# Optimization experiments

Hardware: AMD Instinct MI355X
Metric: run time of the kernel (lower is better)

Reference implementation:

```python
import jax, jax.numpy as jnp
import numpy as np

NEG_SLOPE = 0.2
BN_EPS = 1e-5


def _gat_conv(x, src, dst, W, a_src, a_dst, b, n_nodes):
    # PyG GATConv, heads=1: linear, per-edge leaky-relu score, per-dst softmax, scatter-add.
    h = x @ W  # [N, C]
    e = jax.nn.leaky_relu((h @ a_src)[src] + (h @ a_dst)[dst], NEG_SLOPE)  # [E]
    m = jax.ops.segment_max(e, dst, num_segments=n_nodes)
    m = jnp.where(jnp.isfinite(m), m, 0.0)  # nodes with no in-edges
    w = jnp.exp(e - m[dst])
    denom = jax.ops.segment_sum(w, dst, num_segments=n_nodes)
    alpha = w / (denom[dst] + 1e-16)  # [E]
    out = jax.ops.segment_sum(alpha[:, None] * h[src], dst, num_segments=n_nodes)
    return out + b


def setup_inputs() -> dict:
    key = jax.random.key(0)
    N, E, Q, C = 50000, 800000, 200000, 128
    ks = jax.random.split(key, 12)
    sc = 1.0 / np.sqrt(C)
    d = {
        "embedding": jax.random.normal(ks[0], (N, C), jnp.float32) * 0.1,
        "W1": jax.random.normal(ks[1], (C, C), jnp.float32) * sc,
        "a_src1": jax.random.normal(ks[2], (C,), jnp.float32) * sc,
        "a_dst1": jax.random.normal(ks[3], (C,), jnp.float32) * sc,
        "b1": jnp.zeros((C,), jnp.float32),
        "gamma": jnp.ones((C,), jnp.float32),
        "beta": jnp.zeros((C,), jnp.float32),
        "rmean": jnp.zeros((C,), jnp.float32),
        "rvar": jnp.ones((C,), jnp.float32),
        "W2": jax.random.normal(ks[4], (C, C), jnp.float32) * sc,
        "a_src2": jax.random.normal(ks[5], (C,), jnp.float32) * sc,
        "a_dst2": jax.random.normal(ks[6], (C,), jnp.float32) * sc,
        "b2": jnp.zeros((C,), jnp.float32),
        "Wp1": jax.random.normal(ks[7], (C, C), jnp.float32) * sc,
        "bp1": jnp.zeros((C,), jnp.float32),
        "Wp2": jax.random.normal(ks[8], (C, 1), jnp.float32) * sc,
        "bp2": jnp.zeros((1,), jnp.float32),
        "edge_index": jax.random.randint(ks[9], (2, E), 0, N, jnp.int32),
        "edges": jax.random.randint(ks[10], (2, Q), 0, N, jnp.int32),
    }
    return d


def reference(embedding, W1, a_src1, a_dst1, b1, gamma, beta, rmean, rvar,
              W2, a_src2, a_dst2, b2, Wp1, bp1, Wp2, bp2, edge_index, edges):
    N = embedding.shape[0]
    src, dst = edge_index[0], edge_index[1]
    # conv0 -> BN (eval, running stats) -> ReLU (dropout inactive in eval)
    x = _gat_conv(embedding, src, dst, W1, a_src1, a_dst1, b1, N)
    x = (x - rmean) * jax.lax.rsqrt(rvar + BN_EPS) * gamma + beta
    x = jax.nn.relu(x)
    # final conv
    x = _gat_conv(x, src, dst, W2, a_src2, a_dst2, b2, N)
    # LinkPredictor: elementwise product of endpoint embeddings -> MLP -> sigmoid
    h = x[edges[0]] * x[edges[1]]  # [Q, C]
    h = jax.nn.relu(h @ Wp1 + bp1)
    out = jax.nn.sigmoid(h @ Wp2 + bp2)
    return out[:, 0]
```

## Files before the change

### kernel.cpp

```cpp
#include <hip/hip_runtime.h>
#include <hip/hip_bf16.h>
#include <math.h>
#include <stdint.h>
#include <string.h>

#define NEG_SLOPE 0.2f
#define BN_EPS 1e-5f

typedef __attribute__((ext_vector_type(8))) short short8;
typedef __attribute__((ext_vector_type(4))) float float4v;

static __device__ __forceinline__ unsigned short f2bf(float f) {
    union { float f; unsigned u; } v; v.f = f;
    unsigned r = (v.u + 0x7fffu + ((v.u >> 16) & 1u)) >> 16;
    return (unsigned short)r;
}
static __device__ __forceinline__ float bf2f(unsigned short u) {
    union { unsigned u; float f; } v; v.u = ((unsigned)u) << 16;
    return v.f;
}

__global__ __launch_bounds__(256) void prep_all(
    const float* __restrict__ W1, const float* __restrict__ W2,
    const float* __restrict__ Wp1,
    unsigned short* __restrict__ wt1, unsigned short* __restrict__ wt2,
    unsigned short* __restrict__ wtp,
    const float* __restrict__ gamma, const float* __restrict__ beta,
    const float* __restrict__ rmean, const float* __restrict__ rvar,
    float* __restrict__ bnsc, float* __restrict__ bnsh,
    int* __restrict__ bcur, int nb) {
    int b = blockIdx.x;
    if (b < 192) {
        const float* W = (b < 64) ? W1 : (b < 128) ? W2 : Wp1;
        unsigned short* WT = (b < 64) ? wt1 : (b < 128) ? wt2 : wtp;
        int idx = (b & 63) * 256 + threadIdx.x;
        int k = idx >> 7, n = idx & 127;
        WT[n * 128 + k] = f2bf(W[idx]);
    } else {
        if (threadIdx.x < 128) {
            int c = threadIdx.x;
            float s = gamma[c] * rsqrtf(rvar[c] + BN_EPS);
            bnsc[c] = s;
            bnsh[c] = beta[c] - rmean[c] * s;
        }
        for (int i = threadIdx.x; i < nb; i += 256) bcur[i] = 0;
    }
}

#define BK_CAP 8192
#define BK_EPB 4096
#define BK_LDS 6144

__global__ __launch_bounds__(256) void bucket_scatter(const int* __restrict__ src,
                                                      const int* __restrict__ dst,
                                                      int* __restrict__ bcur,
                                                      unsigned long long* __restrict__ bucket,
                                                      int E) {
    __shared__ int lcnt[256];
    __shared__ int lbase[256];
    int t = threadIdx.x;
    int e0 = blockIdx.x * BK_EPB;
    lcnt[t] = 0;
    __syncthreads();

    int es[16], ed[16];
#pragma unroll
    for (int u = 0; u < 16; ++u) {
        int i = e0 + u * 256 + t;
        if (i < E) {
            es[u] = src[i];
            ed[u] = dst[i];
            atomicAdd(&lcnt[ed[u] >> 8], 1);
        } else {
            ed[u] = -1;
        }
    }
    __syncthreads();
    int c = lcnt[t];
    if (c > 0) lbase[t] = atomicAdd(&bcur[t], c);
    __syncthreads();
    lcnt[t] = 0;
    __syncthreads();
#pragma unroll
    for (int u = 0; u < 16; ++u) {
        if (ed[u] >= 0) {
            int bin = ed[u] >> 8;
            int r = atomicAdd(&lcnt[bin], 1);
            int slot = lbase[bin] + r;
            if (slot < BK_CAP)
                bucket[(size_t)bin * BK_CAP + slot] =
                    ((unsigned long long)(ed[u] & 255) << 32) | (unsigned)es[u];
        }
    }
}

__global__ __launch_bounds__(1024) void scan_bucket_sums(const int* __restrict__ bcur,
                                                         int* __restrict__ bbase,
                                                         int* __restrict__ offs,
                                                         int nb, int N) {
    __shared__ int s[1024];
    int t = threadIdx.x;
    int v = 0;
    if (t < nb) { v = bcur[t]; if (v > BK_CAP) v = BK_CAP; }
    s[t] = v;
    __syncthreads();
    for (int d = 1; d < 1024; d <<= 1) {
        int u = (t >= d) ? s[t - d] : 0;
        __syncthreads();
        s[t] += u;
        __syncthreads();
    }
    if (t < nb) bbase[t] = s[t] - v;
    if (t == 1023) offs[N] = s[1023];
}

__global__ __launch_bounds__(256) void bucket_offs_fill(
    const int* __restrict__ bcur,
    const unsigned long long* __restrict__ bucket,
    const int* __restrict__ bbase,
    int* __restrict__ offs, int* __restrict__ csr, int N) {
    __shared__ unsigned long long rec[BK_LDS];
    __shared__ int cnt[256];
    __shared__ int sc[256];
    int t = threadIdx.x, b = blockIdx.x;
    const unsigned long long* gb = &bucket[(size_t)b * BK_CAP];
    cnt[t] = 0;
    int c = bcur[b];
    if (c > BK_CAP) c = BK_CAP;
    int lim = (c < BK_LDS) ? c : BK_LDS;
    for (int i = t; i < lim; i += 256) rec[i] = gb[i];
    __syncthreads();
    for (int i = t; i < c; i += 256) {
        unsigned long long v = (i < BK_LDS) ? rec[i] : gb[i];
        atomicAdd(&cnt[(int)(v >> 32)], 1);
    }
    __syncthreads();
    int v = cnt[t];
    sc[t] = v;
    __syncthreads();
    for (int d = 1; d < 256; d <<= 1) {
        int u = (t >= d) ? sc[t - d] : 0;
        __syncthreads();
        sc[t] += u;
        __syncthreads();
    }
    int myoff = bbase[b] + sc[t] - v;
    int node = (b << 8) + t;
    if (node < N) offs[node] = myoff;
    cnt[t] = myoff;
    __syncthreads();
    for (int i = t; i < c; i += 256) {
        unsigned long long rv = (i < BK_LDS) ? rec[i] : gb[i];
        int dl = (int)(rv >> 32);
        int s = (int)(rv & 0xffffffffu);
        int r = atomicAdd(&cnt[dl], 1);
        csr[r] = s;
    }
}

#define LP_RS 136

template <bool BF16_IN>
__global__ __launch_bounds__(256) void gemm_mfma(
    const void* __restrict__ Xv,
    const unsigned short* __restrict__ WT,
    const float* __restrict__ a_src, const float* __restrict__ a_dst,
    unsigned short* __restrict__ H,
    float* __restrict__ s_src, float* __restrict__ s_dst, int N)
{
    __shared__ unsigned short sA[128 * LP_RS];
    __shared__ unsigned short sW[128 * LP_RS];
    const float* Xf = (const float*)Xv;
    const unsigned short* Xh = (const unsigned short*)Xv;
    int tid = threadIdx.x;
    int r0 = blockIdx.x * 128;

#pragma unroll
    for (int it = 0; it < 8; ++it) {
        int idx = it * 2048 + tid * 8;
        int n = idx >> 7, k = idx & 127;
        *(short8*)&sW[n * LP_RS + k] = *(const short8*)&WT[idx];
    }
#pragma unroll
    for (int it = 0; it < 16; ++it) {
        int r = it * 8 + (tid >> 5);
        int c = (tid & 31) * 4;
        int row = r0 + r;
        ushort4 u = make_ushort4(0, 0, 0, 0);
        if (row < N) {
            if (BF16_IN) {
                u = *(const ushort4*)&Xh[(size_t)row * 128 + c];
            } else {
                float4 x = *(const float4*)&Xf[(size_t)row * 128 + c];
                u.x = f2bf(x.x); u.y = f2bf(x.y); u.z = f2bf(x.z); u.w = f2bf(x.w);
            }
        }
        *(ushort4*)&sA[r * LP_RS + c] = u;
    }
    __syncthreads();

    int wave = tid >> 6, lane = tid & 63;
    int ln = lane & 15, quad = lane >> 4;
    int rowbase = wave * 32;

    short8 af[2][4];
#pragma unroll
    for (int m = 0; m < 2; ++m)
#pragma unroll
        for (int kt = 0; kt < 4; ++kt)
            af[m][kt] = *(const short8*)&sA[(rowbase + m * 16 + ln) * LP_RS + kt * 32 + quad * 8];

    float4v acc[2][8];
#pragma unroll
    for (int m = 0; m < 2; ++m)
#pragma unroll
        for (int n = 0; n < 8; ++n)
            acc[m][n] = float4v{0.f, 0.f, 0.f, 0.f};

#pragma unroll
    for (int n = 0; n < 8; ++n) {
#pragma unroll
        for (int kt = 0; kt < 4; ++kt) {
            short8 bf = *(const short8*)&sW[(n * 16 + ln) * LP_RS + kt * 32 + quad * 8];
            acc[0][n] = __builtin_amdgcn_mfma_f32_16x16x32_bf16(af[0][kt], bf, acc[0][n], 0, 0, 0);
            acc[1][n] = __builtin_amdgcn_mfma_f32_16x16x32_bf16(af[1][kt], bf, acc[1][n], 0, 0, 0);
        }
    }

    float asr[8], adr[8];
#pragma unroll
    for (int n = 0; n < 8; ++n) {
        asr[n] = a_src[n * 16 + ln];
        adr[n] = a_dst[n * 16 + ln];
    }
#pragma unroll
    for (int m = 0; m < 2; ++m) {
        int rb = r0 + rowbase + m * 16 + quad * 4;
#pragma unroll
        for (int n = 0; n < 8; ++n) {
            int col = n * 16 + ln;
            float4v a = acc[m][n];
            if (rb + 0 < N) H[(size_t)(rb + 0) * 128 + col] = f2bf(a[0]);
            if (rb + 1 < N) H[(size_t)(rb + 1) * 128 + col] = f2bf(a[1]);
            if (rb + 2 < N) H[(size_t)(rb + 2) * 128 + col] = f2bf(a[2]);
            if (rb + 3 < N) H[(size_t)(rb + 3) * 128 + col] = f2bf(a[3]);
        }
#pragma unroll
        for (int r = 0; r < 4; ++r) {
            float ps = 0.f, pd = 0.f;
#pragma unroll
            for (int n = 0; n < 8; ++n) {
                float v = acc[m][n][r];
                ps = fmaf(v, asr[n], ps);
                pd = fmaf(v, adr[n], pd);
            }
#pragma unroll
            for (int o = 1; o < 16; o <<= 1) {
                ps += __shfl_xor(ps, o);
                pd += __shfl_xor(pd, o);
            }
            int row = rb + r;
            if (ln == 0 && row < N) { s_src[row] = ps; s_dst[row] = pd; }
        }
    }
}

__global__ __launch_bounds__(256) void edge_softmax(const int* __restrict__ off,
                                                    const int* __restrict__ csr,
                                                    const float* __restrict__ s_src,
                                                    const float* __restrict__ s_dst,
                                                    float* __restrict__ we,
                                                    float* __restrict__ invd, int N) {
    int tid = threadIdx.x;
    int node = blockIdx.x * 16 + (tid >> 4);
    if (node >= N) return;
    int ln = tid & 15;
    int beg = off[node], end = off[node + 1];
    float sd = s_dst[node];

    float sw = 0.f;
    for (int i = beg + ln; i < end; i += 16) {
        float e = s_src[csr[i]] + sd;
        e = (e >= 0.f) ? e : NEG_SLOPE * e;
        float w = expf(e);
        we[i] = w;
        sw += w;
    }
#pragma unroll
    for (int o = 8; o; o >>= 1) sw += __shfl_xor(sw, o);
    if (ln == 0) invd[node] = 1.f / (sw + 1e-16f);
}

__global__ __launch_bounds__(256) void gat_gather(const unsigned short* __restrict__ H,
                                                  const int* __restrict__ off,
                                                  const int* __restrict__ csr,
                                                  const float* __restrict__ we,
                                                  const float* __restrict__ invd,
                                                  const float* __restrict__ bias,
                                                  const float* __restrict__ bn_scale,
                                                  const float* __restrict__ bn_shift,
                                                  int do_bn_relu,
                                                  unsigned short* __restrict__ out, int N) {
    int wave = threadIdx.x >> 6, lane = threadIdx.x & 63;
    int half = lane >> 5, hl = lane & 31;
    int node = blockIdx.x * 8 + wave * 2 + half;
    if (node >= N) return;
    int c0 = hl * 4;
    int beg = off[node], end = off[node + 1];
    float inv = invd[node];

    float a0 = 0.f, a1 = 0.f, a2 = 0.f, a3 = 0.f;
    int i = beg;
    for (; i + 8 <= end; i += 8) {
        int s[8]; float w[8]; ushort4 hv[8];
#pragma unroll
        for (int u = 0; u < 8; ++u) { s[u] = csr[i + u]; w[u] = we[i + u]; }
#pragma unroll
        for (int u = 0; u < 8; ++u)
            hv[u] = *(const ushort4*)&H[(size_t)s[u] * 128 + c0];
#pragma unroll
        for (int u = 0; u < 8; ++u) {
            a0 = fmaf(w[u], bf2f(hv[u].x), a0);
            a1 = fmaf(w[u], bf2f(hv[u].y), a1);
            a2 = fmaf(w[u], bf2f(hv[u].z), a2);
            a3 = fmaf(w[u], bf2f(hv[u].w), a3);
        }
    }
    for (; i < end; ++i) {
        int s = csr[i];
        float w = we[i];
        ushort4 hv = *(const ushort4*)&H[(size_t)s * 128 + c0];
        a0 = fmaf(w, bf2f(hv.x), a0);
        a1 = fmaf(w, bf2f(hv.y), a1);
        a2 = fmaf(w, bf2f(hv.z), a2);
        a3 = fmaf(w, bf2f(hv.w), a3);
    }
    float o0 = a0 * inv + bias[c0 + 0];
    float o1 = a1 * inv + bias[c0 + 1];
    float o2 = a2 * inv + bias[c0 + 2];
    float o3 = a3 * inv + bias[c0 + 3];
    if (do_bn_relu) {
        o0 = fmaxf(o0 * bn_scale[c0 + 0] + bn_shift[c0 + 0], 0.f);
        o1 = fmaxf(o1 * bn_scale[c0 + 1] + bn_shift[c0 + 1], 0.f);
        o2 = fmaxf(o2 * bn_scale[c0 + 2] + bn_shift[c0 + 2], 0.f);
        o3 = fmaxf(o3 * bn_scale[c0 + 3] + bn_shift[c0 + 3], 0.f);
    }
    ushort4 ov;
    ov.x = f2bf(o0); ov.y = f2bf(o1); ov.z = f2bf(o2); ov.w = f2bf(o3);
    *(ushort4*)&out[(size_t)node * 128 + c0] = ov;
}

__global__ __launch_bounds__(512) void link_pred_mfma(
    const unsigned short* __restrict__ X,
    const int* __restrict__ E0, const int* __restrict__ E1,
    const unsigned short* __restrict__ WTg,
    const float* __restrict__ bp1,
    const float* __restrict__ Wp2,
    const float* __restrict__ bp2_p,
    float* __restrict__ out, int Q)
{
    __shared__ unsigned short sW[128 * LP_RS];
    int tid = threadIdx.x;
    int wave = tid >> 6, lane = tid & 63;
    int ln = lane & 15, quad = lane >> 4;

    int tile = blockIdx.x * 8 + wave;
    int qbase = tile * 32;

    int ea[2], eb[2];
#pragma unroll
    for (int m = 0; m < 2; ++m) {
        int q = qbase + m * 16 + ln;
        if (q >= Q) q = Q - 1;
        ea[m] = E0[q];
        eb[m] = E1[q];
    }

#pragma unroll
    for (int it = 0; it < 4; ++it) {
        int idx = it * 4096 + tid * 8;
        int n = idx >> 7, k = idx & 127;
        *(short8*)&sW[n * LP_RS + k] = *(const short8*)&WTg[idx];
    }

    short8 ra[2][4], rb[2][4];
#pragma unroll
    for (int m = 0; m < 2; ++m) {
        const unsigned short* pa = &X[(size_t)ea[m] * 128 + quad * 8];
        const unsigned short* pb = &X[(size_t)eb[m] * 128 + quad * 8];
#pragma unroll
        for (int kt = 0; kt < 4; ++kt) {
            ra[m][kt] = *(const short8*)(pa + kt * 32);
            rb[m][kt] = *(const short8*)(pb + kt * 32);
        }
    }

    float bias[8], w2c[8];
#pragma unroll
    for (int n = 0; n < 8; ++n) {
        bias[n] = bp1[n * 16 + ln];
        w2c[n] = Wp2[n * 16 + ln];
    }
    float b2 = bp2_p[0];

    __syncthreads();

    short8 af[2][4];
#pragma unroll
    for (int m = 0; m < 2; ++m) {
#pragma unroll
        for (int kt = 0; kt < 4; ++kt) {
            short8 p;
#pragma unroll
            for (int j = 0; j < 8; j += 2) {
                float p0 = bf2f((unsigned short)ra[m][kt][j]) *
                           bf2f((unsigned short)rb[m][kt][j]);
                float p1 = bf2f((unsigned short)ra[m][kt][j + 1]) *
                           bf2f((unsigned short)rb[m][kt][j + 1]);
                __hip_bfloat162 h2 = __float22bfloat162_rn(make_float2(p0, p1));
                unsigned pr;
                memcpy(&pr, &h2, 4);
                p[j]     = (short)(pr & 0xffffu);
                p[j + 1] = (short)(pr >> 16);
            }
            af[m][kt] = p;
        }
    }

    float r0[2] = {0.f, 0.f}, r1[2] = {0.f, 0.f}, r2[2] = {0.f, 0.f}, r3[2] = {0.f, 0.f};
#pragma unroll
    for (int n = 0; n < 8; ++n) {
        float4v a0 = float4v{bias[n], bias[n], bias[n], bias[n]};
        float4v a1 = a0;
#pragma unroll
        for (int kt = 0; kt < 4; ++kt) {
            short8 bf = *(const short8*)&sW[(n * 16 + ln) * LP_RS + kt * 32 + quad * 8];
            a0 = __builtin_amdgcn_mfma_f32_16x16x32_bf16(af[0][kt], bf, a0, 0, 0, 0);
            a1 = __builtin_amdgcn_mfma_f32_16x16x32_bf16(af[1][kt], bf, a1, 0, 0, 0);
        }
        float w = w2c[n];
        r0[0] += fmaxf(a0[0], 0.f) * w;  r0[1] += fmaxf(a1[0], 0.f) * w;
        r1[0] += fmaxf(a0[1], 0.f) * w;  r1[1] += fmaxf(a1[1], 0.f) * w;
        r2[0] += fmaxf(a0[2], 0.f) * w;  r2[1] += fmaxf(a1[2], 0.f) * w;
        r3[0] += fmaxf(a0[3], 0.f) * w;  r3[1] += fmaxf(a1[3], 0.f) * w;
    }
#pragma unroll
    for (int m = 0; m < 2; ++m) {
#pragma unroll
        for (int o = 1; o < 16; o <<= 1) {
            r0[m] += __shfl_xor(r0[m], o);
            r1[m] += __shfl_xor(r1[m], o);
            r2[m] += __shfl_xor(r2[m], o);
            r3[m] += __shfl_xor(r3[m], o);
        }
        if (ln == 0) {
            int rbase = qbase + m * 16 + quad * 4;
            float rv[4] = {r0[m], r1[m], r2[m], r3[m]};
#pragma unroll
            for (int r = 0; r < 4; ++r) {
                int q = rbase + r;
                if (q < Q) out[q] = 1.f / (1.f + expf(-(rv[r] + b2)));
            }
        }
    }
}

extern "C" void kernel_launch(void* const* d_in, const int* in_sizes, int n_in,
                              void* d_out, int out_size, void* d_ws, size_t ws_size,
                              hipStream_t stream) {
    const float* emb    = (const float*)d_in[0];
    const float* W1     = (const float*)d_in[1];
    const float* a_src1 = (const float*)d_in[2];
    const float* a_dst1 = (const float*)d_in[3];
    const float* b1     = (const float*)d_in[4];
    const float* gamma  = (const float*)d_in[5];
    const float* beta   = (const float*)d_in[6];
    const float* rmean  = (const float*)d_in[7];
    const float* rvar   = (const float*)d_in[8];
    const float* W2     = (const float*)d_in[9];
    const float* a_src2 = (const float*)d_in[10];
    const float* a_dst2 = (const float*)d_in[11];
    const float* b2     = (const float*)d_in[12];
    const float* Wp1    = (const float*)d_in[13];
    const float* bp1    = (const float*)d_in[14];
    const float* Wp2    = (const float*)d_in[15];
    const float* bp2    = (const float*)d_in[16];
    const int* edge_index = (const int*)d_in[17];
    const int* edges      = (const int*)d_in[18];

    const int N = in_sizes[0] / 128;
    const int E = in_sizes[17] / 2;
    const int Q = in_sizes[18] / 2;
    const int* src = edge_index;
    const int* dst = edge_index + E;
    const int* e0 = edges;
    const int* e1 = edges + Q;
    float* out = (float*)d_out;

    uintptr_t base = (uintptr_t)d_ws;
    size_t cur = 0;
    auto take = [&](size_t bytes) -> void* {
        void* p = (void*)(base + cur);
        cur += (bytes + 255) & ~(size_t)255;
        return p;
    };
    unsigned short* bufA = (unsigned short*)take((size_t)N * 128 * 2);
    unsigned short* bufB = (unsigned short*)take((size_t)N * 128 * 2);
    float* s_src  = (float*)take((size_t)N * 4);
    float* s_dst  = (float*)take((size_t)N * 4);
    float* bnsc   = (float*)take(128 * 4);
    float* bnsh   = (float*)take(128 * 4);
    int*   offs   = (int*)take((size_t)(N + 1) * 4);
    int*   csr    = (int*)take((size_t)E * 4);
    float* we     = (float*)take((size_t)E * 4);
    float* invd   = (float*)take((size_t)N * 4);
    unsigned short* wt1 = (unsigned short*)take(128 * 128 * 2);
    unsigned short* wt2 = (unsigned short*)take(128 * 128 * 2);
    unsigned short* wtp = (unsigned short*)take(128 * 128 * 2);
    int nb = (N + 255) / 256;
    int*   bcur   = (int*)take((size_t)nb * 4);
    int*   bbase  = (int*)take((size_t)nb * 4);
    unsigned long long* bucket =
        (unsigned long long*)take((size_t)nb * BK_CAP * 8);
    (void)ws_size; (void)n_in; (void)out_size;

    prep_all<<<193, 256, 0, stream>>>(W1, W2, Wp1, wt1, wt2, wtp,
                                      gamma, beta, rmean, rvar, bnsc, bnsh,
                                      bcur, nb);

    bucket_scatter<<<(E + BK_EPB - 1) / BK_EPB, 256, 0, stream>>>(src, dst, bcur, bucket, E);
    scan_bucket_sums<<<1, 1024, 0, stream>>>(bcur, bbase, offs, nb, N);
    bucket_offs_fill<<<nb, 256, 0, stream>>>(bcur, bucket, bbase, offs, csr, N);

    int gblk = (N + 127) / 128;
    gemm_mfma<false><<<gblk, 256, 0, stream>>>(emb, wt1, a_src1, a_dst1, bufA, s_src, s_dst, N);
    edge_softmax<<<(N + 15) / 16, 256, 0, stream>>>(offs, csr, s_src, s_dst, we, invd, N);
    gat_gather<<<(N + 7) / 8, 256, 0, stream>>>(bufA, offs, csr, we, invd, b1,
                                                bnsc, bnsh, 1, bufB, N);
    gemm_mfma<true><<<gblk, 256, 0, stream>>>(bufB, wt2, a_src2, a_dst2, bufA, s_src, s_dst, N);
    edge_softmax<<<(N + 15) / 16, 256, 0, stream>>>(offs, csr, s_src, s_dst, we, invd, N);
    gat_gather<<<(N + 7) / 8, 256, 0, stream>>>(bufA, offs, csr, we, invd, b2,
                                                nullptr, nullptr, 0, bufB, N);
    int ntiles = (Q + 31) / 32;
    int lblk = (ntiles + 7) / 8;
    link_pred_mfma<<<lblk, 512, 0, stream>>>(bufB, e0, e1, wtp, bp1, Wp2, bp2, out, Q);
}
```

Baseline: 272.2 us.

## Fuse edge softmax into GAT gather and replace bucket scan with atomic base

The separate edge_softmax kernel is removed. The gather kernel now computes edge weights on the fly, one edge per lane in chunks of 32, broadcasts index and weight by shuffle, and reduces the denominator in-warp. This drops the per-edge weight array write and read plus two launches. The single-block scan kernel is replaced by an atomicAdd on a global counter inside bucket_offs_fill. That makes per-bucket CSR segments non-contiguous, so an explicit ends array is added. Shuffle overhead and exp work now sit on the gather's critical path.

```diff
diff --git a/kernel.cpp b/kernel.cpp
--- a/kernel.cpp
+++ b/kernel.cpp
@@ -28,7 +28,7 @@
     const float* __restrict__ gamma, const float* __restrict__ beta,
     const float* __restrict__ rmean, const float* __restrict__ rvar,
     float* __restrict__ bnsc, float* __restrict__ bnsh,
-    int* __restrict__ bcur, int nb) {
+    int* __restrict__ bcur, int nz) {
     int b = blockIdx.x;
     if (b < 192) {
         const float* W = (b < 64) ? W1 : (b < 128) ? W2 : Wp1;
@@ -43,7 +43,7 @@
             bnsc[c] = s;
             bnsh[c] = beta[c] - rmean[c] * s;
         }
-        for (int i = threadIdx.x; i < nb; i += 256) bcur[i] = 0;
+        for (int i = threadIdx.x; i < nz; i += 256) bcur[i] = 0;
     }
 }
 
@@ -94,39 +94,22 @@
     }
 }
 
-__global__ __launch_bounds__(1024) void scan_bucket_sums(const int* __restrict__ bcur,
-                                                         int* __restrict__ bbase,
-                                                         int* __restrict__ offs,
-                                                         int nb, int N) {
-    __shared__ int s[1024];
-    int t = threadIdx.x;
-    int v = 0;
-    if (t < nb) { v = bcur[t]; if (v > BK_CAP) v = BK_CAP; }
-    s[t] = v;
-    __syncthreads();
-    for (int d = 1; d < 1024; d <<= 1) {
-        int u = (t >= d) ? s[t - d] : 0;
-        __syncthreads();
-        s[t] += u;
-        __syncthreads();
-    }
-    if (t < nb) bbase[t] = s[t] - v;
-    if (t == 1023) offs[N] = s[1023];
-}
-
 __global__ __launch_bounds__(256) void bucket_offs_fill(
     const int* __restrict__ bcur,
     const unsigned long long* __restrict__ bucket,
-    const int* __restrict__ bbase,
-    int* __restrict__ offs, int* __restrict__ csr, int N) {
+    int* __restrict__ gcnt,
+    int* __restrict__ offs, int* __restrict__ ends,
+    int* __restrict__ csr, int N) {
     __shared__ unsigned long long rec[BK_LDS];
     __shared__ int cnt[256];
     __shared__ int sc[256];
+    __shared__ int bbase;
     int t = threadIdx.x, b = blockIdx.x;
     const unsigned long long* gb = &bucket[(size_t)b * BK_CAP];
     cnt[t] = 0;
     int c = bcur[b];
     if (c > BK_CAP) c = BK_CAP;
+    if (t == 0) bbase = atomicAdd(gcnt, c);
     int lim = (c < BK_LDS) ? c : BK_LDS;
     for (int i = t; i < lim; i += 256) rec[i] = gb[i];
     __syncthreads();
@@ -144,9 +127,12 @@
         sc[t] += u;
         __syncthreads();
     }
-    int myoff = bbase[b] + sc[t] - v;
+    int myoff = bbase + sc[t] - v;
     int node = (b << 8) + t;
-    if (node < N) offs[node] = myoff;
+    if (node < N) {
+        offs[node] = myoff;
+        ends[node] = myoff + v;
+    }
     cnt[t] = myoff;
     __syncthreads();
     for (int i = t; i < c; i += 256) {
@@ -265,37 +251,12 @@
     }
 }
 
-__global__ __launch_bounds__(256) void edge_softmax(const int* __restrict__ off,
-                                                    const int* __restrict__ csr,
-                                                    const float* __restrict__ s_src,
-                                                    const float* __restrict__ s_dst,
-                                                    float* __restrict__ we,
-                                                    float* __restrict__ invd, int N) {
-    int tid = threadIdx.x;
-    int node = blockIdx.x * 16 + (tid >> 4);
-    if (node >= N) return;
-    int ln = tid & 15;
-    int beg = off[node], end = off[node + 1];
-    float sd = s_dst[node];
-
-    float sw = 0.f;
-    for (int i = beg + ln; i < end; i += 16) {
-        float e = s_src[csr[i]] + sd;
-        e = (e >= 0.f) ? e : NEG_SLOPE * e;
-        float w = expf(e);
-        we[i] = w;
-        sw += w;
-    }
-#pragma unroll
-    for (int o = 8; o; o >>= 1) sw += __shfl_xor(sw, o);
-    if (ln == 0) invd[node] = 1.f / (sw + 1e-16f);
-}
-
 __global__ __launch_bounds__(256) void gat_gather(const unsigned short* __restrict__ H,
-                                                  const int* __restrict__ off,
+                                                  const int* __restrict__ offs,
+                                                  const int* __restrict__ ends,
                                                   const int* __restrict__ csr,
-                                                  const float* __restrict__ we,
-                                                  const float* __restrict__ invd,
+                                                  const float* __restrict__ s_src,
+                                                  const float* __restrict__ s_dst,
                                                   const float* __restrict__ bias,
                                                   const float* __restrict__ bn_scale,
                                                   const float* __restrict__ bn_shift,
@@ -306,35 +267,75 @@
     int node = blockIdx.x * 8 + wave * 2 + half;
     if (node >= N) return;
     int c0 = hl * 4;
-    int beg = off[node], end = off[node + 1];
-    float inv = invd[node];
+    int beg = offs[node], end = ends[node];
+    float sd = s_dst[node];
 
     float a0 = 0.f, a1 = 0.f, a2 = 0.f, a3 = 0.f;
-    int i = beg;
-    for (; i + 8 <= end; i += 8) {
-        int s[8]; float w[8]; ushort4 hv[8];
-#pragma unroll
-        for (int u = 0; u < 8; ++u) { s[u] = csr[i + u]; w[u] = we[i + u]; }
-#pragma unroll
-        for (int u = 0; u < 8; ++u)
-            hv[u] = *(const ushort4*)&H[(size_t)s[u] * 128 + c0];
-#pragma unroll
-        for (int u = 0; u < 8; ++u) {
-            a0 = fmaf(w[u], bf2f(hv[u].x), a0);
-            a1 = fmaf(w[u], bf2f(hv[u].y), a1);
-            a2 = fmaf(w[u], bf2f(hv[u].z), a2);
-            a3 = fmaf(w[u], bf2f(hv[u].w), a3);
-        }
-    }
-    for (; i < end; ++i) {
-        int s = csr[i];
-        float w = we[i];
-        ushort4 hv = *(const ushort4*)&H[(size_t)s * 128 + c0];
-        a0 = fmaf(w, bf2f(hv.x), a0);
-        a1 = fmaf(w, bf2f(hv.y), a1);
-        a2 = fmaf(w, bf2f(hv.z), a2);
-        a3 = fmaf(w, bf2f(hv.w), a3);
-    }
+    float sw = 0.f;
+    for (int chunk = beg; chunk < end; chunk += 32) {
+        int i = chunk + hl;
+        int sidx = 0;
+        float w = 0.f;
+        if (i < end) {
+            sidx = csr[i];
+            float e = s_src[sidx] + sd;
+            e = (e >= 0.f) ? e : NEG_SLOPE * e;
+            w = expf(e);
+        }
+        sw += w;
+        int cnt = end - chunk;
+        if (cnt > 32) cnt = 32;
+        int u = 0;
+        for (; u + 8 <= cnt; u += 8) {
+            int s[8]; float ww[8]; ushort4 hv[8];
+#pragma unroll
+            for (int j = 0; j < 8; ++j) {
+                s[j]  = __shfl(sidx, u + j, 32);
+                ww[j] = __shfl(w, u + j, 32);
+            }
+#pragma unroll
+            for (int j = 0; j < 8; ++j)
+                hv[j] = *(const ushort4*)&H[(size_t)s[j] * 128 + c0];
+#pragma unroll
+            for (int j = 0; j < 8; ++j) {
+                a0 = fmaf(ww[j], bf2f(hv[j].x), a0);
+                a1 = fmaf(ww[j], bf2f(hv[j].y), a1);
+                a2 = fmaf(ww[j], bf2f(hv[j].z), a2);
+                a3 = fmaf(ww[j], bf2f(hv[j].w), a3);
+            }
+        }
+        for (; u + 4 <= cnt; u += 4) {
+            int s[4]; float ww[4]; ushort4 hv[4];
+#pragma unroll
+            for (int j = 0; j < 4; ++j) {
+                s[j]  = __shfl(sidx, u + j, 32);
+                ww[j] = __shfl(w, u + j, 32);
+            }
+#pragma unroll
+            for (int j = 0; j < 4; ++j)
+                hv[j] = *(const ushort4*)&H[(size_t)s[j] * 128 + c0];
+#pragma unroll
+            for (int j = 0; j < 4; ++j) {
+                a0 = fmaf(ww[j], bf2f(hv[j].x), a0);
+                a1 = fmaf(ww[j], bf2f(hv[j].y), a1);
+                a2 = fmaf(ww[j], bf2f(hv[j].z), a2);
+                a3 = fmaf(ww[j], bf2f(hv[j].w), a3);
+            }
+        }
+        for (; u < cnt; ++u) {
+            int sj = __shfl(sidx, u, 32);
+            float wj = __shfl(w, u, 32);
+            ushort4 hv = *(const ushort4*)&H[(size_t)sj * 128 + c0];
+            a0 = fmaf(wj, bf2f(hv.x), a0);
+            a1 = fmaf(wj, bf2f(hv.y), a1);
+            a2 = fmaf(wj, bf2f(hv.z), a2);
+            a3 = fmaf(wj, bf2f(hv.w), a3);
+        }
+    }
+#pragma unroll
+    for (int o = 16; o; o >>= 1) sw += __shfl_xor(sw, o);
+    float inv = 1.f / (sw + 1e-16f);
+
     float o0 = a0 * inv + bias[c0 + 0];
     float o1 = a1 * inv + bias[c0 + 1];
     float o2 = a2 * inv + bias[c0 + 2];
@@ -510,37 +511,32 @@
     float* s_dst  = (float*)take((size_t)N * 4);
     float* bnsc   = (float*)take(128 * 4);
     float* bnsh   = (float*)take(128 * 4);
-    int*   offs   = (int*)take((size_t)(N + 1) * 4);
+    int*   offs   = (int*)take((size_t)N * 4);
+    int*   ends   = (int*)take((size_t)N * 4);
     int*   csr    = (int*)take((size_t)E * 4);
-    float* we     = (float*)take((size_t)E * 4);
-    float* invd   = (float*)take((size_t)N * 4);
     unsigned short* wt1 = (unsigned short*)take(128 * 128 * 2);
     unsigned short* wt2 = (unsigned short*)take(128 * 128 * 2);
     unsigned short* wtp = (unsigned short*)take(128 * 128 * 2);
     int nb = (N + 255) / 256;
-    int*   bcur   = (int*)take((size_t)nb * 4);
-    int*   bbase  = (int*)take((size_t)nb * 4);
+    int*   bcur   = (int*)take((size_t)(nb + 1) * 4);
     unsigned long long* bucket =
         (unsigned long long*)take((size_t)nb * BK_CAP * 8);
     (void)ws_size; (void)n_in; (void)out_size;
 
     prep_all<<<193, 256, 0, stream>>>(W1, W2, Wp1, wt1, wt2, wtp,
                                       gamma, beta, rmean, rvar, bnsc, bnsh,
-                                      bcur, nb);
+                                      bcur, nb + 1);
 
     bucket_scatter<<<(E + BK_EPB - 1) / BK_EPB, 256, 0, stream>>>(src, dst, bcur, bucket, E);
-    scan_bucket_sums<<<1, 1024, 0, stream>>>(bcur, bbase, offs, nb, N);
-    bucket_offs_fill<<<nb, 256, 0, stream>>>(bcur, bucket, bbase, offs, csr, N);
+    bucket_offs_fill<<<nb, 256, 0, stream>>>(bcur, bucket, &bcur[nb], offs, ends, csr, N);
 
     int gblk = (N + 127) / 128;
     gemm_mfma<false><<<gblk, 256, 0, stream>>>(emb, wt1, a_src1, a_dst1, bufA, s_src, s_dst, N);
-    edge_softmax<<<(N + 15) / 16, 256, 0, stream>>>(offs, csr, s_src, s_dst, we, invd, N);
-    gat_gather<<<(N + 7) / 8, 256, 0, stream>>>(bufA, offs, csr, we, invd, b1,
-                                                bnsc, bnsh, 1, bufB, N);
+    gat_gather<<<(N + 7) / 8, 256, 0, stream>>>(bufA, offs, ends, csr, s_src, s_dst,
+                                                b1, bnsc, bnsh, 1, bufB, N);
     gemm_mfma<true><<<gblk, 256, 0, stream>>>(bufB, wt2, a_src2, a_dst2, bufA, s_src, s_dst, N);
-    edge_softmax<<<(N + 15) / 16, 256, 0, stream>>>(offs, csr, s_src, s_dst, we, invd, N);
-    gat_gather<<<(N + 7) / 8, 256, 0, stream>>>(bufA, offs, csr, we, invd, b2,
-                                                nullptr, nullptr, 0, bufB, N);
+    gat_gather<<<(N + 7) / 8, 256, 0, stream>>>(bufA, offs, ends, csr, s_src, s_dst,
+                                                b2, nullptr, nullptr, 0, bufB, N);
     int ntiles = (Q + 31) / 32;
     int lblk = (ntiles + 7) / 8;
     link_pred_mfma<<<lblk, 512, 0, stream>>>(bufB, e0, e1, wtp, bp1, Wp2, bp2, out, Q);
```

Result: faster. 248.0 us (-8.9%).
